# Kernel optimization log

Hardware: AMD Instinct MI355X
Metric: run time of the kernel (lower is better)

The kernel has to match this reference:

```python
import jax, jax.numpy as jnp
import numpy as np

NG, CPN, K = 16, 24, 5          # ngroups, channels-per-group, kernel size
C = NG * CPN                     # 384 total channels
PAD = K // 2                     # PseudoEntropyPad(2, ...)


def build_mask():
    """PixelCNN-style group-causal mask for MaskConv2 (hidden/type-B: center
    position allows input group <= output group)."""
    m = np.zeros((C, C, K, K), np.float32)
    m[:, :, :PAD, :] = 1.0                      # rows above center: all allowed
    m[:, :, PAD, :PAD] = 1.0                    # center row, left of center
    g = np.arange(C) // CPN
    m[:, :, PAD, PAD] = (g[None, :] <= g[:, None]).astype(np.float32)
    return jnp.asarray(m)


def masked_conv(x, w, b, mask):
    # zero pad by 2 (PseudoEntropyPad) + VALID 5x5 conv == SAME conv
    y = jax.lax.conv_general_dilated(
        x, w * mask, window_strides=(1, 1), padding=[(PAD, PAD), (PAD, PAD)],
        dimension_numbers=("NCHW", "OIHW", "NCHW"))
    return y + b[None, :, None, None]


def prelu(x, a):
    return jnp.where(x >= 0, x, a[None, :, None, None] * x)


def setup_inputs() -> dict:
    key = jax.random.key(0)
    ks = jax.random.split(key, 5)
    x = jax.random.normal(ks[0], (2, C, 256, 512), dtype=jnp.float32)
    w1 = jax.random.normal(ks[1], (C, C, K, K), dtype=jnp.float32) * 0.02
    w2 = jax.random.normal(ks[2], (C, C, K, K), dtype=jnp.float32) * 0.02
    b1 = jnp.zeros((C,), jnp.float32)
    b2 = jnp.zeros((C,), jnp.float32)
    a1 = jnp.full((C,), 0.25, jnp.float32)   # PReLU init
    a2 = jnp.full((C,), 0.25, jnp.float32)
    return {"x": x, "w1": w1, "b1": b1, "a1": a1, "w2": w2, "b2": b2, "a2": a2}


def reference(x, w1, b1, a1, w2, b2, a2):
    mask = build_mask()
    y = prelu(masked_conv(x, w1, b1, mask), a1)   # EntropyConv 1 (pad+conv+PReLU+trim)
    y = prelu(masked_conv(y, w2, b2, mask), a2)   # EntropyConv 2
    return y + x                                   # residual
```

## Files before the change

kernel.cpp:

```cpp
#include <hip/hip_runtime.h>
#include <hip/hip_bf16.h>


#define C_CH 384
#define HH   256
#define WWD  512
#define NN   2
#define NKC  24
#define PR   260
#define PC   516
#define ICS16 (PR * PC * 16)
#define TCOLS 144
#define PLANE_SH (4 * TCOLS * 16)
#define TSH (2 * PLANE_SH)
#define TSTRIDE (NKC * C_CH * 16)
#define ICSTRIDE (2 * C_CH * 16)

typedef __attribute__((ext_vector_type(8)))  short short8;
typedef __attribute__((ext_vector_type(16))) float f32x16;

typedef const __attribute__((address_space(1))) void* gas_t;
typedef __attribute__((address_space(3))) void* las_t;

__device__ inline unsigned short f2bf(float f) {
    union { float f; unsigned int u; } v; v.f = f;
    unsigned int r = v.u + 0x7FFFu + ((v.u >> 16) & 1u);
    return (unsigned short)(r >> 16);
}

__global__ __launch_bounds__(256) void k_prepack(const float* __restrict__ w1, const float* __restrict__ w2,
                                                 unsigned short* __restrict__ wp1, unsigned short* __restrict__ wp2) {
    int idx = blockIdx.x * 256 + threadIdx.x;
    const int TOT = 13 * NKC * C_CH * 16;
    if (idx >= TOT) return;
    int iq = idx & 15;
    int o  = (idx >> 4) % C_CH;
    int kc = (idx / (16 * C_CH)) % NKC;
    int t  = idx / (16 * C_CH * NKC);
    int i  = kc * 16 + iq;
    int kh = t < 5 ? 0 : (t < 10 ? 1 : 2);
    int kw = t < 5 ? t : (t < 10 ? t - 5 : t - 10);
    bool keep = (t != 12) || ((i / 24) <= (o / 24));
    int src = ((o * C_CH + i) * 5 + kh) * 5 + kw;
    wp1[idx] = keep ? f2bf(w1[src]) : (unsigned short)0;
    wp2[idx] = keep ? f2bf(w2[src]) : (unsigned short)0;
}

__global__ __launch_bounds__(256) void k_zero_halo(unsigned short* __restrict__ a, unsigned short* __restrict__ b) {
    int plane = blockIdx.x;
    const short8 z = (short8){0,0,0,0,0,0,0,0};
    for (int bi = 0; bi < 2; ++bi) {
        unsigned short* p = (bi ? b : a) + (size_t)plane * ICS16;
        for (int i = threadIdx.x; i < 4128; i += 256) {
            int r4 = i / 1032;
            int rem = i - r4 * 1032;
            int row = r4 < 2 ? r4 : 254 + r4;
            *(short8*)&p[row * (PC * 16) + rem * 8] = z;
        }
        for (int i = threadIdx.x; i < 2048; i += 256) {
            int row = 2 + (i >> 3);
            int j = i & 7;
            int col = (j < 4) ? (j >> 1) : (512 + (j >> 1));
            int q = j & 1;
            *(short8*)&p[(row * PC + col) * 16 + q * 8] = z;
        }
    }
}

__global__ __launch_bounds__(256) void k_repack_x(const float* __restrict__ x, unsigned short* __restrict__ xc) {
    int bid = blockIdx.x;
    int w0 = (bid & 7) << 6;
    int h  = (bid >> 3) & 255;
    int n  = bid >> 11;
    int wi = threadIdx.x & 63;
    int cq = threadIdx.x >> 6;
    int w  = w0 + wi;
    int inb = n * C_CH * HH * WWD + h * WWD + w;
    for (int cc = 0; cc < 12; ++cc) {
        int c0 = cc * 32 + cq * 8;
        short8 outv;
        #pragma unroll
        for (int k = 0; k < 8; ++k) {
            float f = x[inb + (c0 + k) * (HH * WWD)];
            outv[k] = (short)f2bf(f);
        }
        int kc = cc * 2 + (cq >> 1);
        int oidx = (n * NKC + kc) * ICS16 + ((h + 2) * PC + (w + 2)) * 16 + (cq & 1) * 8;
        *(short8*)&xc[oidx] = outv;
    }
}

template<int SECOND>
__global__ __launch_bounds__(256, 2) void k_conv(const unsigned short* __restrict__ in,
                                                 const unsigned short* __restrict__ wp,
                                                 const float* __restrict__ bias,
                                                 const float* __restrict__ alpha,
                                                 const float* __restrict__ xres,
                                                 void* __restrict__ outp) {
    __shared__ __align__(16) unsigned short Xs[2][TSH];

    int bid0 = blockIdx.x;
    int xcd = bid0 & 7;
    int j0  = bid0 >> 3;
    int tile = xcd * 128 + j0 / 3;
    int ob   = j0 % 3;
    int n    = tile >> 9;
    int hp   = (tile >> 2) & 127;
    int wseg = tile & 3;
    int w0 = wseg << 7, o0 = ob << 7, h0 = hp << 1;

    int tid = threadIdx.x;
    int lane = tid & 63;
    int wv = tid >> 6;
    int wr = wv >> 1, wc = wv & 1;
    int lo5 = lane & 31, hi = lane >> 5;

    int goff[9];
    #pragma unroll
    for (int it = 0; it < 9; ++it) {
        int k = wv * 9 + it;
        int plane = k / 18;
        int s = (k % 18) * 64 + lane;
        int r = s / 288;
        int rem = s - r * 288;
        int col = rem >> 1, h16 = rem & 1;
        goff[it] = plane * ICS16 + ((h0 + r) * PC + (w0 + col)) * 16 + h16 * 8;
    }

    f32x16 acc[4][2];
    #pragma unroll
    for (int pt = 0; pt < 4; ++pt)
        #pragma unroll
        for (int ot = 0; ot < 2; ++ot)
            #pragma unroll
            for (int r = 0; r < 16; ++r) acc[pt][ot][r] = 0.f;

    const unsigned short* gbase_n = in + (size_t)n * NKC * ICS16;

    const int xlane = wr * (TCOLS * 16) + lo5 * 16 + hi * 8;
    const unsigned short* wpb = wp + (size_t)(o0 + wc * 64) * 16;
    const int wlane = lo5 * 16 + hi * 8;
    int woff0 = 0;
    int woff1 = C_CH * 16;

    const int KH[13] = {0,0,0,0,0,1,1,1,1,1,2,2,2};
    const int KW[13] = {0,1,2,3,4,0,1,2,3,4,0,1,2};

#define LOAD_XG(dst, u) do {                                              \
        const int s_ = (u) >> 1, ph_ = (u) & 1;                           \
        const int t_ = s_ >> 1, hf_ = s_ & 1;                             \
        const int c0_ = hf_ * PLANE_SH + KH[t_] * (TCOLS * 16)            \
                      + KW[t_] * 16 + ph_ * 1024;                         \
        (dst)[0] = *(const short8*)&xsp[xlane + c0_];                     \
        (dst)[1] = *(const short8*)&xsp[xlane + c0_ + 512];               \
    } while (0)

#define LOAD_WB(dst, woff) do {                                           \
        (dst)[0] = *(const short8*)&wpb[(woff) + wlane];                  \
        (dst)[1] = *(const short8*)&wpb[(woff) + wlane + 512];            \
    } while (0)

    short8 wb[2][2];
    LOAD_WB(wb[0], woff0);
    LOAD_WB(wb[1], woff1);

    #pragma unroll
    for (int it = 0; it < 9; ++it)
        __builtin_amdgcn_global_load_lds((gas_t)(gbase_n + goff[it]),
                                         (las_t)&Xs[0][(wv * 9 + it) * 512], 16, 0, 0);
    __syncthreads();

    for (int ic = 0; ic < 12; ++ic) {
        const unsigned short* xsp = &Xs[ic & 1][0];
        if (ic < 11) {
            const unsigned short* gb = gbase_n + (size_t)(ic + 1) * 2 * ICS16;
            #pragma unroll
            for (int it = 0; it < 9; ++it)
                __builtin_amdgcn_global_load_lds((gas_t)(gb + goff[it]),
                                                 (las_t)&Xs[(ic & 1) ^ 1][(wv * 9 + it) * 512], 16, 0, 0);
        }

        const bool live12 = !((ob == 0 && ic >= 5) || (ob == 1 && ic >= 9));

        short8 xg[4][2];
        LOAD_XG(xg[0], 0);
        LOAD_XG(xg[1], 1);
        LOAD_XG(xg[2], 2);

        #pragma unroll
        for (int g = 0; g < 52; ++g) {
            if (g + 3 < 52) LOAD_XG(xg[(g + 3) & 3], g + 3);
            if ((g & 1) == 0) {
                __builtin_amdgcn_s_barrier();
                __builtin_amdgcn_s_setprio(1);
            }
            if (g < 48 || live12) {
                const int pt0 = (g & 1) * 2;
                #pragma unroll
                for (int pi = 0; pi < 2; ++pi)
                    #pragma unroll
                    for (int ot = 0; ot < 2; ++ot) {
                        if (SECOND)
                            acc[pt0 + pi][ot] = __builtin_amdgcn_mfma_f32_32x32x16_bf16(
                                wb[(g >> 1) & 1][ot], xg[g & 3][pi], acc[pt0 + pi][ot], 0, 0, 0);
                        else
                            acc[pt0 + pi][ot] = __builtin_amdgcn_mfma_f32_32x32x16_bf16(
                                xg[g & 3][pi], wb[(g >> 1) & 1][ot], acc[pt0 + pi][ot], 0, 0, 0);
                    }
            }
            if ((g & 1) == 1) {
                __builtin_amdgcn_s_setprio(0);
                const int s2 = g >> 1;
                if (s2 + 2 < 26) {
                    if ((s2 & 1) == 0) { woff0 += TSTRIDE; LOAD_WB(wb[0], woff0); }
                    else               { woff1 += TSTRIDE; LOAD_WB(wb[1], woff1); }
                } else {
                    if ((s2 & 1) == 0) { woff0 += ICSTRIDE - 12 * TSTRIDE; LOAD_WB(wb[0], woff0); }
                    else               { woff1 += ICSTRIDE - 12 * TSTRIDE; LOAD_WB(wb[1], woff1); }
                }
            }
        }
        __syncthreads();
    }
#undef LOAD_XG
#undef LOAD_WB

    int h = h0 + wr;
    if (!SECOND) {
        unsigned short* y = (unsigned short*)outp;
        #pragma unroll
        for (int ot = 0; ot < 2; ++ot) {
            int o = o0 + wc * 64 + ot * 32 + lo5;
            float bo = bias[o], ao = alpha[o];
            int kc = o >> 4;
            int o15 = o & 15;
            size_t base = (size_t)(n * NKC + kc) * ICS16 + ((h + 2) * PC + (w0 + 2)) * 16 + o15;
            #pragma unroll
            for (int pt = 0; pt < 4; ++pt) {
                #pragma unroll
                for (int reg = 0; reg < 16; ++reg) {
                    int p = pt * 32 + (reg & 3) + 8 * (reg >> 2) + 4 * hi;
                    float v = acc[pt][ot][reg] + bo;
                    v = v >= 0.f ? v : ao * v;
                    y[base + (size_t)p * 16] = f2bf(v);
                }
            }
        }
    } else {
        float* outf = (float*)outp;
        #pragma unroll
        for (int ot = 0; ot < 2; ++ot) {
            #pragma unroll
            for (int reg = 0; reg < 16; ++reg) {
                int o = o0 + wc * 64 + ot * 32 + (reg & 3) + 8 * (reg >> 2) + 4 * hi;
                float bo = bias[o], ao = alpha[o];
                #pragma unroll
                for (int pt = 0; pt < 4; ++pt) {
                    int w = w0 + pt * 32 + lo5;
                    float v = acc[pt][ot][reg] + bo;
                    v = v >= 0.f ? v : ao * v;
                    size_t idx = (size_t)((n * C_CH + o) * HH + h) * WWD + w;
                    outf[idx] = v + xres[idx];
                }
            }
        }
    }
}

extern "C" void kernel_launch(void* const* d_in, const int* in_sizes, int n_in,
                              void* d_out, int out_size, void* d_ws, size_t ws_size,
                              hipStream_t stream) {
    const float* x  = (const float*)d_in[0];
    const float* w1 = (const float*)d_in[1];
    const float* b1 = (const float*)d_in[2];
    const float* a1 = (const float*)d_in[3];
    const float* w2 = (const float*)d_in[4];
    const float* b2 = (const float*)d_in[5];
    const float* a2 = (const float*)d_in[6];

    const size_t PLANE_SHORTS = (size_t)NN * NKC * ICS16;
    unsigned short* xc  = (unsigned short*)d_out;
    unsigned short* yb  = (unsigned short*)d_ws;
    unsigned short* wp1 = yb + PLANE_SHORTS;
    unsigned short* wp2 = wp1 + 13 * NKC * C_CH * 16;

    k_prepack<<<(13 * NKC * C_CH * 16 + 255) / 256, 256, 0, stream>>>(w1, w2, wp1, wp2);
    k_zero_halo<<<NN * NKC, 256, 0, stream>>>(xc, yb);
    k_repack_x<<<NN * HH * (WWD / 64), 256, 0, stream>>>(x, xc);
    k_conv<0><<<3072, 256, 0, stream>>>(xc, wp1, b1, a1, nullptr, (void*)yb);
    k_conv<1><<<3072, 256, 0, stream>>>(yb, wp2, b2, a2, x, (void*)d_out);
}
```

Baseline: 1.781 ms.

## Merge two conv tiles into one 512-thread block with ping-pong MFMA phases

Each block now has two 4-wave groups, each owning a two-row tile with its own double-buffered LDS slice. The groups alternate between MFMA work and LDS/weight loads through s_barrier-separated phases, so one group's matrix work overlaps the other's memory traffic, replacing the previous 2-blocks-per-CU scheduling. This costs more barriers per iteration, and the register budget at one 512-thread block per CU may differ from before.

```diff
diff --git a/kernel.cpp b/kernel.cpp
--- a/kernel.cpp
+++ b/kernel.cpp
@@ -91,34 +91,37 @@
 }
 
 template<int SECOND>
-__global__ __launch_bounds__(256, 2) void k_conv(const unsigned short* __restrict__ in,
+__global__ __launch_bounds__(512, 1) void k_conv(const unsigned short* __restrict__ in,
                                                  const unsigned short* __restrict__ wp,
                                                  const float* __restrict__ bias,
                                                  const float* __restrict__ alpha,
                                                  const float* __restrict__ xres,
                                                  void* __restrict__ outp) {
-    __shared__ __align__(16) unsigned short Xs[2][TSH];
+    __shared__ __align__(16) unsigned short Xs[2][2][TSH];
 
     int bid0 = blockIdx.x;
     int xcd = bid0 & 7;
     int j0  = bid0 >> 3;
-    int tile = xcd * 128 + j0 / 3;
+    int tile = xcd * 64 + j0 / 3;
     int ob   = j0 % 3;
-    int n    = tile >> 9;
-    int hp   = (tile >> 2) & 127;
+    int n    = tile >> 8;
+    int hq   = (tile >> 2) & 63;
     int wseg = tile & 3;
-    int w0 = wseg << 7, o0 = ob << 7, h0 = hp << 1;
+    int w0 = wseg << 7, o0 = ob << 7;
 
     int tid = threadIdx.x;
     int lane = tid & 63;
     int wv = tid >> 6;
-    int wr = wv >> 1, wc = wv & 1;
+    int grp = wv >> 2;
+    int wvg = wv & 3;
+    int wr = wvg >> 1, wc = wvg & 1;
     int lo5 = lane & 31, hi = lane >> 5;
+    int h0 = (hq << 2) + grp * 2;
 
     int goff[9];
     #pragma unroll
     for (int it = 0; it < 9; ++it) {
-        int k = wv * 9 + it;
+        int k = wvg * 9 + it;
         int plane = k / 18;
         int s = (k % 18) * 64 + lane;
         int r = s / 288;
@@ -160,6 +163,38 @@
         (dst)[1] = *(const short8*)&wpb[(woff) + wlane + 512];            \
     } while (0)
 
+#define GRANULE(g) do {                                                   \
+        const int pt0_ = ((g) & 1) * 2;                                   \
+        _Pragma("unroll")                                                 \
+        for (int pi = 0; pi < 2; ++pi)                                    \
+            _Pragma("unroll")                                             \
+            for (int ot = 0; ot < 2; ++ot) {                              \
+                if (SECOND)                                               \
+                    acc[pt0_ + pi][ot] = __builtin_amdgcn_mfma_f32_32x32x16_bf16( \
+                        wb[((g) >> 1) & 1][ot], xg[(g) & 3][pi], acc[pt0_ + pi][ot], 0, 0, 0); \
+                else                                                      \
+                    acc[pt0_ + pi][ot] = __builtin_amdgcn_mfma_f32_32x32x16_bf16( \
+                        xg[(g) & 3][pi], wb[((g) >> 1) & 1][ot], acc[pt0_ + pi][ot], 0, 0, 0); \
+            }                                                             \
+    } while (0)
+
+#define PHASE_WORK(c) do {                                                \
+        __builtin_amdgcn_s_setprio(1);                                    \
+        if ((c) < 24 || live12) { GRANULE(2*(c)); GRANULE(2*(c)+1); }     \
+        __builtin_amdgcn_s_setprio(0);                                    \
+        if ((c) < 24) {                                                   \
+            LOAD_XG(xg[(2*(c)+4) & 3], 2*(c)+4);                          \
+            LOAD_XG(xg[(2*(c)+5) & 3], 2*(c)+5);                          \
+        }                                                                 \
+        if ((c) + 2 < 26) {                                               \
+            if (((c) & 1) == 0) { woff0 += TSTRIDE; LOAD_WB(wb[0], woff0); } \
+            else                { woff1 += TSTRIDE; LOAD_WB(wb[1], woff1); } \
+        } else {                                                          \
+            if (((c) & 1) == 0) { woff0 += ICSTRIDE - 12 * TSTRIDE; LOAD_WB(wb[0], woff0); } \
+            else                { woff1 += ICSTRIDE - 12 * TSTRIDE; LOAD_WB(wb[1], woff1); } \
+        }                                                                 \
+    } while (0)
+
     short8 wb[2][2];
     LOAD_WB(wb[0], woff0);
     LOAD_WB(wb[1], woff1);
@@ -167,17 +202,17 @@
     #pragma unroll
     for (int it = 0; it < 9; ++it)
         __builtin_amdgcn_global_load_lds((gas_t)(gbase_n + goff[it]),
-                                         (las_t)&Xs[0][(wv * 9 + it) * 512], 16, 0, 0);
+                                         (las_t)&Xs[grp][0][(wvg * 9 + it) * 512], 16, 0, 0);
     __syncthreads();
 
     for (int ic = 0; ic < 12; ++ic) {
-        const unsigned short* xsp = &Xs[ic & 1][0];
+        const unsigned short* xsp = &Xs[grp][ic & 1][0];
         if (ic < 11) {
             const unsigned short* gb = gbase_n + (size_t)(ic + 1) * 2 * ICS16;
             #pragma unroll
             for (int it = 0; it < 9; ++it)
                 __builtin_amdgcn_global_load_lds((gas_t)(gb + goff[it]),
-                                                 (las_t)&Xs[(ic & 1) ^ 1][(wv * 9 + it) * 512], 16, 0, 0);
+                                                 (las_t)&Xs[grp][(ic & 1) ^ 1][(wvg * 9 + it) * 512], 16, 0, 0);
         }
 
         const bool live12 = !((ob == 0 && ic >= 5) || (ob == 1 && ic >= 9));
@@ -186,44 +221,21 @@
         LOAD_XG(xg[0], 0);
         LOAD_XG(xg[1], 1);
         LOAD_XG(xg[2], 2);
-
-        #pragma unroll
-        for (int g = 0; g < 52; ++g) {
-            if (g + 3 < 52) LOAD_XG(xg[(g + 3) & 3], g + 3);
-            if ((g & 1) == 0) {
-                __builtin_amdgcn_s_barrier();
-                __builtin_amdgcn_s_setprio(1);
-            }
-            if (g < 48 || live12) {
-                const int pt0 = (g & 1) * 2;
-                #pragma unroll
-                for (int pi = 0; pi < 2; ++pi)
-                    #pragma unroll
-                    for (int ot = 0; ot < 2; ++ot) {
-                        if (SECOND)
-                            acc[pt0 + pi][ot] = __builtin_amdgcn_mfma_f32_32x32x16_bf16(
-                                wb[(g >> 1) & 1][ot], xg[g & 3][pi], acc[pt0 + pi][ot], 0, 0, 0);
-                        else
-                            acc[pt0 + pi][ot] = __builtin_amdgcn_mfma_f32_32x32x16_bf16(
-                                xg[g & 3][pi], wb[(g >> 1) & 1][ot], acc[pt0 + pi][ot], 0, 0, 0);
-                    }
-            }
-            if ((g & 1) == 1) {
-                __builtin_amdgcn_s_setprio(0);
-                const int s2 = g >> 1;
-                if (s2 + 2 < 26) {
-                    if ((s2 & 1) == 0) { woff0 += TSTRIDE; LOAD_WB(wb[0], woff0); }
-                    else               { woff1 += TSTRIDE; LOAD_WB(wb[1], woff1); }
-                } else {
-                    if ((s2 & 1) == 0) { woff0 += ICSTRIDE - 12 * TSTRIDE; LOAD_WB(wb[0], woff0); }
-                    else               { woff1 += ICSTRIDE - 12 * TSTRIDE; LOAD_WB(wb[1], woff1); }
-                }
-            }
+        LOAD_XG(xg[3], 3);
+
+        #pragma unroll
+        for (int c = 0; c < 26; ++c) {
+            __builtin_amdgcn_s_barrier();
+            if (grp == 0) PHASE_WORK(c);
+            __builtin_amdgcn_s_barrier();
+            if (grp == 1) PHASE_WORK(c);
         }
         __syncthreads();
     }
 #undef LOAD_XG
 #undef LOAD_WB
+#undef GRANULE
+#undef PHASE_WORK
 
     int h = h0 + wr;
     if (!SECOND) {
@@ -287,6 +299,6 @@
     k_prepack<<<(13 * NKC * C_CH * 16 + 255) / 256, 256, 0, stream>>>(w1, w2, wp1, wp2);
     k_zero_halo<<<NN * NKC, 256, 0, stream>>>(xc, yb);
     k_repack_x<<<NN * HH * (WWD / 64), 256, 0, stream>>>(x, xc);
-    k_conv<0><<<3072, 256, 0, stream>>>(xc, wp1, b1, a1, nullptr, (void*)yb);
-    k_conv<1><<<3072, 256, 0, stream>>>(yb, wp2, b2, a2, x, (void*)d_out);
-}
+    k_conv<0><<<1536, 512, 0, stream>>>(xc, wp1, b1, a1, nullptr, (void*)yb);
+    k_conv<1><<<1536, 512, 0, stream>>>(yb, wp2, b2, a2, x, (void*)d_out);
+}
```

Measured after the change: 2.001 ms. 12.4% more time.
